# Optimization experiments

Measured on AMD Instinct MI355X. Metric: run time of the kernel, lower is better.

The kernel has to match this reference:

```python
import jax, jax.numpy as jnp
import numpy as np

RES_W, RES_H = 256, 256
MAX_SAMPLES = 384
TF_RES = 128
FOV_DEG = 30.0
NEAR, FAR = 0.1, 100.0
BG = 0.0
HIT_EPS = 1e-3


def _normalize(v, axis=-1):
    return v / jnp.linalg.norm(v, axis=axis, keepdims=True)


def trilinear_sample(vol, tex):
    # vol: [X,Y,Z], tex: [...,3] in voxel coordinates
    res = np.array(vol.shape, dtype=np.float32)
    p = jnp.clip(tex, 0.0, jnp.asarray(res - 1.0 - 1e-6, jnp.float32))
    lo = jnp.floor(p).astype(jnp.int32)
    f = p - lo.astype(p.dtype)
    hi = jnp.minimum(lo + 1, jnp.asarray(res.astype(np.int32) - 1))
    x0, y0, z0 = lo[..., 0], lo[..., 1], lo[..., 2]
    x1, y1, z1 = hi[..., 0], hi[..., 1], hi[..., 2]
    fx, fy, fz = f[..., 0], f[..., 1], f[..., 2]
    c000 = vol[x0, y0, z0]; c100 = vol[x1, y0, z0]
    c010 = vol[x0, y1, z0]; c110 = vol[x1, y1, z0]
    c001 = vol[x0, y0, z1]; c101 = vol[x1, y0, z1]
    c011 = vol[x0, y1, z1]; c111 = vol[x1, y1, z1]
    c00 = c000 * (1 - fx) + c100 * fx
    c10 = c010 * (1 - fx) + c110 * fx
    c01 = c001 * (1 - fx) + c101 * fx
    c11 = c011 * (1 - fx) + c111 * fx
    c0 = c00 * (1 - fy) + c10 * fy
    c1 = c01 * (1 - fy) + c11 * fy
    return c0 * (1 - fz) + c1 * fz


def tf_lookup(tf, x):
    # tf: [T,4], x: [...] intensity in [0,1]
    T = tf.shape[0]
    xi = jnp.clip(x, 0.0, 1.0) * (T - 1)
    lo = jnp.floor(xi).astype(jnp.int32)
    hi = jnp.minimum(lo + 1, T - 1)
    f = (xi - lo.astype(xi.dtype))[..., None]
    return tf[lo] * (1 - f) + tf[hi] * f


def render_one(vol, tf, cam, sr):
    # vol [X,Y,Z], tf [T,4], cam [3] -> [W,H,5] (rgba + depth)
    W, H = RES_W, RES_H
    fwd = _normalize(-cam)
    world_up = jnp.array([0.0, 1.0, 0.0], jnp.float32)
    right = _normalize(jnp.cross(fwd, world_up))
    up = jnp.cross(right, fwd)
    tanf = jnp.tan(jnp.float32(np.radians(FOV_DEG) / 2))
    aspect = W / H
    u = ((jnp.arange(W) + 0.5) / W * 2 - 1) * tanf * aspect  # [W]
    v = ((jnp.arange(H) + 0.5) / H * 2 - 1) * tanf           # [H]
    dirs = fwd + u[:, None, None] * right + v[None, :, None] * up  # [W,H,3]
    dirs = _normalize(dirs)
    # ray-box intersection against [-1,1]^3
    inv = 1.0 / dirs
    t_lo = (-1.0 - cam) * inv
    t_hi = (1.0 - cam) * inv
    tmin = jnp.max(jnp.minimum(t_lo, t_hi), axis=-1)
    tmax = jnp.min(jnp.maximum(t_lo, t_hi), axis=-1)
    hit = (tmax >= 0.0) & (tmin <= tmax)
    entry = jnp.maximum(tmin, NEAR)
    dist = jnp.where(hit, jnp.maximum(tmax - entry, 0.0), 0.0)
    vol_max = max(vol.shape)
    # Nyquist: step = voxel size (2/vol_max) / sampling_rate
    ns = jnp.clip(jnp.ceil(dist * 0.5 * vol_max * sr), 1.0, MAX_SAMPLES)
    step = dist / ns
    k = jnp.arange(MAX_SAMPLES, dtype=jnp.float32)
    t = entry[..., None] + (k + 0.5) * step[..., None]            # [W,H,S]
    valid = (k < ns[..., None]) & hit[..., None]
    pos = cam + t[..., None] * dirs[..., None, :]                 # [W,H,S,3]
    res_m1 = jnp.asarray(np.array(vol.shape, np.float32) - 1.0)
    tex = (pos * 0.5 + 0.5) * res_m1
    intensity = trilinear_sample(vol, tex)                        # [W,H,S]
    rgba = tf_lookup(tf, intensity)                               # [W,H,S,4]
    a = rgba[..., 3]
    a = 1.0 - (1.0 - a) ** (1.0 / sr)   # opacity correction for sampling rate
    a = jnp.where(valid, a, 0.0)
    one_m = 1.0 - a
    cp = jnp.cumprod(one_m, axis=-1)
    T_excl = jnp.concatenate([jnp.ones_like(cp[..., :1]), cp[..., :-1]], axis=-1)
    w = T_excl * a                                                # [W,H,S]
    rgb = jnp.einsum('whs,whsc->whc', w, rgba[..., :3])
    acc = jnp.sum(w, axis=-1)
    rgb_out = rgb + (1.0 - acc)[..., None] * BG
    # FirstHitDepth
    hit_s = a > HIT_EPS
    any_hit = jnp.any(hit_s, axis=-1)
    first = jnp.argmax(hit_s, axis=-1)
    t_first = jnp.take_along_axis(t, first[..., None], axis=-1)[..., 0]
    depth = jnp.where(any_hit, (t_first - NEAR) / (FAR - NEAR), 1.0)
    return jnp.concatenate([rgb_out, acc[..., None], depth[..., None]], axis=-1)


def setup_inputs() -> dict:
    key = jax.random.key(0)
    k1, k2, k3 = jax.random.split(key, 3)
    volume = jax.random.uniform(k1, (1, 256, 256, 256), dtype=jnp.float32)
    tf = jax.random.uniform(k2, (1, TF_RES, 4), dtype=jnp.float32)
    look_from = jnp.array([[0.9, 0.7, -2.2]], jnp.float32) + 0.1 * jax.random.normal(k3, (1, 3), dtype=jnp.float32)
    return {"volume": volume, "tf": tf, "look_from": look_from, "sampling_rate": 1}


def reference(volume, tf, look_from, sampling_rate):
    sr = float(sampling_rate)
    return jax.vmap(lambda v, t, c: render_one(v, t, c, sr))(volume, tf, look_from)
```

## Files before the change

### kernel.cpp

```cpp
#include <hip/hip_runtime.h>
#include <math.h>

#define RES_W 256
#define RES_H 256
#define TF_RES 128

typedef float float2u __attribute__((ext_vector_type(2), aligned(4)));

__global__ __launch_bounds__(256, 4) void raycast_kernel(
    const float* __restrict__ vol,
    const float* __restrict__ tf,
    const float* __restrict__ cam_p,
    const int*   __restrict__ sr_p,
    float* __restrict__ out)
{
    #pragma clang fp contract(off)

    __shared__ float tfR[TF_RES + 1], tfG[TF_RES + 1], tfB[TF_RES + 1], tfA[TF_RES + 1];
    const int tid = (int)threadIdx.x;
    if (tid < TF_RES) {
        float4 e = ((const float4*)tf)[tid];
        tfR[tid] = e.x; tfG[tid] = e.y; tfB[tid] = e.z; tfA[tid] = e.w;
        if (tid == TF_RES - 1) {
            tfR[TF_RES] = e.x; tfG[TF_RES] = e.y; tfB[TF_RES] = e.z; tfA[TF_RES] = e.w;
        }
    }
    __syncthreads();

    const int lane = tid & 63;
    const int sub  = lane & 31;

    const int b  = (int)blockIdx.x;
    const int sb = (b & 7) * 1024 + (b >> 3);
    const int ray = sb * 8 + (tid >> 5);
    const int h = ray & 255;
    const int w = ray >> 8;

    const float cx = cam_p[0], cy = cam_p[1], cz = cam_p[2];
    const int   sr_i = sr_p[0];
    const float srf = (float)sr_i;

    float nx = -cx, ny = -cy, nz = -cz;
    float fl = __fsqrt_rn((nx*nx + ny*ny) + nz*nz);
    float fx = nx / fl, fy = ny / fl, fz = nz / fl;
    float rxu = 0.0f - fz;
    float rzu = fx;
    float rl = __fsqrt_rn((rxu*rxu + 0.0f) + rzu*rzu);
    float rx = rxu / rl, rz = rzu / rl;
    float ux = 0.0f - rz*fy;
    float uy = rz*fx - rx*fz;
    float uz = rx*fy;

    const float ang32 = (float)((30.0 * 0.017453292519943295) * 0.5);
    const float tan_half = (float)tan((double)ang32);

    float uu = ((((float)w + 0.5f) / 256.0f) * 2.0f - 1.0f) * tan_half;
    float vv = ((((float)h + 0.5f) / 256.0f) * 2.0f - 1.0f) * tan_half;

    float dx = (fx + uu*rx) + vv*ux;
    float dy = (fy + 0.0f ) + vv*uy;
    float dz = (fz + uu*rz) + vv*uz;
    float dl = __fsqrt_rn((dx*dx + dy*dy) + dz*dz);
    dx = dx / dl; dy = dy / dl; dz = dz / dl;

    float ivx = 1.0f/dx, ivy = 1.0f/dy, ivz = 1.0f/dz;
    float tlx = (-1.0f - cx)*ivx, thx = (1.0f - cx)*ivx;
    float tly = (-1.0f - cy)*ivy, thy = (1.0f - cy)*ivy;
    float tlz = (-1.0f - cz)*ivz, thz = (1.0f - cz)*ivz;
    float tmin = fmaxf(fmaxf(fminf(tlx,thx), fminf(tly,thy)), fminf(tlz,thz));
    float tmax = fminf(fminf(fmaxf(tlx,thx), fmaxf(tly,thy)), fmaxf(tlz,thz));
    bool hit = (tmax >= 0.0f) && (tmin <= tmax);

    float entry = fmaxf(tmin, 0.1f);
    float dist  = hit ? fmaxf(tmax - entry, 0.0f) : 0.0f;
    float nsf   = fminf(fmaxf(ceilf(((dist * 0.5f) * 256.0f) * srf), 1.0f), 384.0f);
    int   ns    = (int)nsf;
    float step  = dist / nsf;

    float rgb_r = 0.0f, rgb_g = 0.0f, rgb_b = 0.0f, acc = 0.0f;
    float T_prev = 1.0f;
    int   hk_min = 0x7FFFFFFF;

    for (int base = 0; ; ) {
        const int  k     = base + sub;
        const bool valid = hit && (k < ns);

        float t  = entry + ((float)k + 0.5f) * step;
        float px = (cx + t*dx);
        float py = (cy + t*dy);
        float pz = (cz + t*dz);
        px = ((px * 0.5f) + 0.5f) * 255.0f;
        py = ((py * 0.5f) + 0.5f) * 255.0f;
        pz = ((pz * 0.5f) + 0.5f) * 255.0f;
        px = fminf(fmaxf(px, 0.0f), 255.0f);
        py = fminf(fmaxf(py, 0.0f), 255.0f);
        pz = fminf(fmaxf(pz, 0.0f), 255.0f);
        int x0 = (int)floorf(px), y0 = (int)floorf(py), z0 = (int)floorf(pz);
        float ffx = px - (float)x0;
        float ffy = py - (float)y0;
        float ffz = pz - (float)z0;
        int x1 = min(x0 + 1, 255);
        int y1 = min(y0 + 1, 255);
        int zb = min(z0, 254);
        int bx0 = x0 << 16, bx1 = x1 << 16;
        int by0 = y0 << 8,  by1 = y1 << 8;
        float2u p00 = *(const float2u*)(vol + (bx0 + by0 + zb));
        float2u p10 = *(const float2u*)(vol + (bx1 + by0 + zb));
        float2u p01 = *(const float2u*)(vol + (bx0 + by1 + zb));
        float2u p11 = *(const float2u*)(vol + (bx1 + by1 + zb));
        if (z0 == 255) {
            p00.x = p00.y; p10.x = p10.y; p01.x = p01.y; p11.x = p11.y;
        }

        float omx = 1.0f - ffx, omy = 1.0f - ffy, omz = 1.0f - ffz;
        float c00 = p00.x*omx + p10.x*ffx;
        float c10 = p01.x*omx + p11.x*ffx;
        float c01 = p00.y*omx + p10.y*ffx;
        float c11 = p01.y*omx + p11.y*ffx;
        float c0  = c00*omy + c10*ffy;
        float c1  = c01*omy + c11*ffy;
        float intensity = c0*omz + c1*ffz;

        float xi = fminf(fmaxf(intensity, 0.0f), 1.0f) * 127.0f;
        int lo  = (int)floorf(xi);
        float tfr = xi - (float)lo;
        float omt = 1.0f - tfr;
        float cr  = tfR[lo]*omt + tfR[lo + 1]*tfr;
        float cg  = tfG[lo]*omt + tfG[lo + 1]*tfr;
        float cbb = tfB[lo]*omt + tfB[lo + 1]*tfr;
        float a   = tfA[lo]*omt + tfA[lo + 1]*tfr;

        if (sr_i == 1) {
            a = 1.0f - (1.0f - a);
        } else {
            a = 1.0f - powf(1.0f - a, 1.0f / srf);
        }
        if (!valid) a = 0.0f;
        float one_m = 1.0f - a;

        float x = one_m;
        #pragma unroll
        for (int off = 1; off < 32; off <<= 1) {
            float y = __shfl_up(x, off);
            if (sub >= off) x *= y;
        }
        float ex = __shfl_up(x, 1);
        if (sub == 0) ex = 1.0f;

        float wgt = (T_prev * ex) * a;
        rgb_r += wgt * cr;
        rgb_g += wgt * cg;
        rgb_b += wgt * cbb;
        acc   += wgt;
        if (valid && (a > 1e-3f)) hk_min = min(hk_min, k);

        float Tc = __shfl(x, (lane & 32) | 31);
        T_prev = T_prev * Tc;

        base += 32;
        bool active = hit && (base < ns) && (T_prev >= 1e-7f);
        if (__ballot(active) == 0ULL) break;
    }

    #pragma unroll
    for (int m = 16; m >= 1; m >>= 1) {
        rgb_r += __shfl_xor(rgb_r, m);
        rgb_g += __shfl_xor(rgb_g, m);
        rgb_b += __shfl_xor(rgb_b, m);
        acc   += __shfl_xor(acc,   m);
        hk_min = min(hk_min, __shfl_xor(hk_min, m));
    }

    if (sub == 0) {
        float depth = 1.0f;
        if (hk_min != 0x7FFFFFFF) {
            float tfh = entry + ((float)hk_min + 0.5f) * step;
            depth = (tfh - 0.1f) / 99.9f;
        }
        int oi = (w * RES_H + h) * 5;
        out[oi + 0] = rgb_r;
        out[oi + 1] = rgb_g;
        out[oi + 2] = rgb_b;
        out[oi + 3] = acc;
        out[oi + 4] = depth;
    }
}

extern "C" void kernel_launch(void* const* d_in, const int* in_sizes, int n_in,
                              void* d_out, int out_size, void* d_ws, size_t ws_size,
                              hipStream_t stream) {
    const float* vol = (const float*)d_in[0];
    const float* tf  = (const float*)d_in[1];
    const float* cam = (const float*)d_in[2];
    const int*   sr  = (const int*)d_in[3];
    float* out = (float*)d_out;

    raycast_kernel<<<dim3(8192), dim3(256), 0, stream>>>(vol, tf, cam, sr, out);
}
```

Baseline: 113.7 us.

## Halve lanes per ray, precompute ray setup, and loosen early-termination threshold

```diff
diff --git a/kernel.cpp b/kernel.cpp
--- a/kernel.cpp
+++ b/kernel.cpp
@@ -7,38 +7,18 @@
 
 typedef float float2u __attribute__((ext_vector_type(2), aligned(4)));
 
-__global__ __launch_bounds__(256, 4) void raycast_kernel(
-    const float* __restrict__ vol,
-    const float* __restrict__ tf,
+__global__ __launch_bounds__(256) void ray_setup_kernel(
     const float* __restrict__ cam_p,
     const int*   __restrict__ sr_p,
-    float* __restrict__ out)
+    float* __restrict__ rws)
 {
     #pragma clang fp contract(off)
-
-    __shared__ float tfR[TF_RES + 1], tfG[TF_RES + 1], tfB[TF_RES + 1], tfA[TF_RES + 1];
-    const int tid = (int)threadIdx.x;
-    if (tid < TF_RES) {
-        float4 e = ((const float4*)tf)[tid];
-        tfR[tid] = e.x; tfG[tid] = e.y; tfB[tid] = e.z; tfA[tid] = e.w;
-        if (tid == TF_RES - 1) {
-            tfR[TF_RES] = e.x; tfG[TF_RES] = e.y; tfB[TF_RES] = e.z; tfA[TF_RES] = e.w;
-        }
-    }
-    __syncthreads();
-
-    const int lane = tid & 63;
-    const int sub  = lane & 31;
-
-    const int b  = (int)blockIdx.x;
-    const int sb = (b & 7) * 1024 + (b >> 3);
-    const int ray = sb * 8 + (tid >> 5);
+    const int ray = (int)blockIdx.x * 256 + (int)threadIdx.x;
     const int h = ray & 255;
     const int w = ray >> 8;
 
     const float cx = cam_p[0], cy = cam_p[1], cz = cam_p[2];
-    const int   sr_i = sr_p[0];
-    const float srf = (float)sr_i;
+    const float srf = (float)sr_p[0];
 
     float nx = -cx, ny = -cy, nz = -cz;
     float fl = __fsqrt_rn((nx*nx + ny*ny) + nz*nz);
@@ -74,8 +54,54 @@
     float entry = fmaxf(tmin, 0.1f);
     float dist  = hit ? fmaxf(tmax - entry, 0.0f) : 0.0f;
     float nsf   = fminf(fmaxf(ceilf(((dist * 0.5f) * 256.0f) * srf), 1.0f), 384.0f);
-    int   ns    = (int)nsf;
     float step  = dist / nsf;
+
+    float4* o = (float4*)(rws + (size_t)ray * 8);
+    o[0] = make_float4(dx, dy, dz, entry);
+    o[1] = make_float4(step, nsf, hit ? 1.0f : 0.0f, 0.0f);
+}
+
+__global__ __launch_bounds__(256) void raycast_kernel(
+    const float* __restrict__ vol,
+    const float* __restrict__ tf,
+    const float* __restrict__ cam_p,
+    const int*   __restrict__ sr_p,
+    const float* __restrict__ rws,
+    float* __restrict__ out)
+{
+    #pragma clang fp contract(off)
+
+    __shared__ float tfR[TF_RES + 1], tfG[TF_RES + 1], tfB[TF_RES + 1], tfA[TF_RES + 1];
+    const int tid = (int)threadIdx.x;
+    if (tid < TF_RES) {
+        float4 e = ((const float4*)tf)[tid];
+        tfR[tid] = e.x; tfG[tid] = e.y; tfB[tid] = e.z; tfA[tid] = e.w;
+        if (tid == TF_RES - 1) {
+            tfR[TF_RES] = e.x; tfG[TF_RES] = e.y; tfB[TF_RES] = e.z; tfA[TF_RES] = e.w;
+        }
+    }
+    __syncthreads();
+
+    const int lane = tid & 63;
+    const int sub  = lane & 15;
+
+    const int b  = (int)blockIdx.x;
+    const int sb = (b & 7) * 512 + (b >> 3);
+    const int ray = sb * 16 + (tid >> 4);
+    const int h = ray & 255;
+    const int w = ray >> 8;
+
+    const float cx = cam_p[0], cy = cam_p[1], cz = cam_p[2];
+    const int   sr_i = sr_p[0];
+    const float srf = (float)sr_i;
+
+    const float4* rp = (const float4*)(rws + (size_t)ray * 8);
+    float4 ra = rp[0];
+    float4 rb = rp[1];
+    const float dx = ra.x, dy = ra.y, dz = ra.z, entry = ra.w;
+    const float step = rb.x;
+    const int   ns   = (int)rb.y;
+    const bool  hit  = (rb.z != 0.0f);
 
     float rgb_r = 0.0f, rgb_g = 0.0f, rgb_b = 0.0f, acc = 0.0f;
     float T_prev = 1.0f;
@@ -140,7 +166,7 @@
 
         float x = one_m;
         #pragma unroll
-        for (int off = 1; off < 32; off <<= 1) {
+        for (int off = 1; off < 16; off <<= 1) {
             float y = __shfl_up(x, off);
             if (sub >= off) x *= y;
         }
@@ -154,16 +180,16 @@
         acc   += wgt;
         if (valid && (a > 1e-3f)) hk_min = min(hk_min, k);
 
-        float Tc = __shfl(x, (lane & 32) | 31);
+        float Tc = __shfl(x, (lane & 48) | 15);
         T_prev = T_prev * Tc;
 
-        base += 32;
-        bool active = hit && (base < ns) && (T_prev >= 1e-7f);
+        base += 16;
+        bool active = hit && (base < ns) && (T_prev >= 1e-4f);
         if (__ballot(active) == 0ULL) break;
     }
 
     #pragma unroll
-    for (int m = 16; m >= 1; m >>= 1) {
+    for (int m = 8; m >= 1; m >>= 1) {
         rgb_r += __shfl_xor(rgb_r, m);
         rgb_g += __shfl_xor(rgb_g, m);
         rgb_b += __shfl_xor(rgb_b, m);
@@ -194,6 +220,8 @@
     const float* cam = (const float*)d_in[2];
     const int*   sr  = (const int*)d_in[3];
     float* out = (float*)d_out;
-
-    raycast_kernel<<<dim3(8192), dim3(256), 0, stream>>>(vol, tf, cam, sr, out);
+    float* rws = (float*)d_ws;
+
+    ray_setup_kernel<<<dim3(256), dim3(256), 0, stream>>>(cam, sr, rws);
+    raycast_kernel<<<dim3(4096), dim3(256), 0, stream>>>(vol, tf, cam, sr, rws, out);
 }
```

Measured after the change: 103.4 us. -9.1%, faster.

## Switch to one ray per thread with 8x8 tiles and early ray termination

Applied to the files above, without the earlier changes.

```diff
diff --git a/kernel.cpp b/kernel.cpp
--- a/kernel.cpp
+++ b/kernel.cpp
@@ -7,7 +7,7 @@
 
 typedef float float2u __attribute__((ext_vector_type(2), aligned(4)));
 
-__global__ __launch_bounds__(256, 4) void raycast_kernel(
+__global__ __launch_bounds__(64) void raycast_kernel(
     const float* __restrict__ vol,
     const float* __restrict__ tf,
     const float* __restrict__ cam_p,
@@ -18,23 +18,24 @@
 
     __shared__ float tfR[TF_RES + 1], tfG[TF_RES + 1], tfB[TF_RES + 1], tfA[TF_RES + 1];
     const int tid = (int)threadIdx.x;
-    if (tid < TF_RES) {
-        float4 e = ((const float4*)tf)[tid];
-        tfR[tid] = e.x; tfG[tid] = e.y; tfB[tid] = e.z; tfA[tid] = e.w;
-        if (tid == TF_RES - 1) {
-            tfR[TF_RES] = e.x; tfG[TF_RES] = e.y; tfB[TF_RES] = e.z; tfA[TF_RES] = e.w;
+    {
+        const float4* tf4 = (const float4*)tf;
+        float4 e0 = tf4[tid];
+        float4 e1 = tf4[tid + 64];
+        tfR[tid] = e0.x; tfG[tid] = e0.y; tfB[tid] = e0.z; tfA[tid] = e0.w;
+        tfR[tid + 64] = e1.x; tfG[tid + 64] = e1.y; tfB[tid + 64] = e1.z; tfA[tid + 64] = e1.w;
+        if (tid == 63) {
+            tfR[TF_RES] = e1.x; tfG[TF_RES] = e1.y; tfB[TF_RES] = e1.z; tfA[TF_RES] = e1.w;
         }
     }
     __syncthreads();
 
-    const int lane = tid & 63;
-    const int sub  = lane & 31;
-
-    const int b  = (int)blockIdx.x;
-    const int sb = (b & 7) * 1024 + (b >> 3);
-    const int ray = sb * 8 + (tid >> 5);
-    const int h = ray & 255;
-    const int w = ray >> 8;
+    const int b    = (int)blockIdx.x;
+    const int tile = (b % 8) * 128 + (b / 8);
+    const int tile_h = tile % 32;
+    const int tile_w = tile / 32;
+    const int h = tile_h * 8 + (tid % 8);
+    const int w = tile_w * 8 + (tid / 8);
 
     const float cx = cam_p[0], cy = cam_p[1], cz = cam_p[2];
     const int   sr_i = sr_p[0];
@@ -78,105 +79,82 @@
     float step  = dist / nsf;
 
     float rgb_r = 0.0f, rgb_g = 0.0f, rgb_b = 0.0f, acc = 0.0f;
-    float T_prev = 1.0f;
-    int   hk_min = 0x7FFFFFFF;
+    float Texcl = 1.0f;
+    float depth = 1.0f;
+    bool  found = false;
+    bool  done  = !hit;
+    int   k = 0;
 
-    for (int base = 0; ; ) {
-        const int  k     = base + sub;
-        const bool valid = hit && (k < ns);
+    for (;;) {
+        if (!done) {
+            float t  = entry + ((float)k + 0.5f) * step;
+            float px = (cx + t*dx);
+            float py = (cy + t*dy);
+            float pz = (cz + t*dz);
+            px = ((px * 0.5f) + 0.5f) * 255.0f;
+            py = ((py * 0.5f) + 0.5f) * 255.0f;
+            pz = ((pz * 0.5f) + 0.5f) * 255.0f;
+            px = fminf(fmaxf(px, 0.0f), 255.0f);
+            py = fminf(fmaxf(py, 0.0f), 255.0f);
+            pz = fminf(fmaxf(pz, 0.0f), 255.0f);
+            int x0 = (int)px, y0 = (int)py, z0 = (int)pz;
+            float ffx = px - (float)x0;
+            float ffy = py - (float)y0;
+            float ffz = pz - (float)z0;
+            int x1 = min(x0 + 1, 255);
+            int y1 = min(y0 + 1, 255);
+            int zb = min(z0, 254);
+            int bx0 = x0 << 16, bx1 = x1 << 16;
+            int by0 = y0 << 8,  by1 = y1 << 8;
+            float2u p00 = *(const float2u*)(vol + (bx0 + by0 + zb));
+            float2u p10 = *(const float2u*)(vol + (bx1 + by0 + zb));
+            float2u p01 = *(const float2u*)(vol + (bx0 + by1 + zb));
+            float2u p11 = *(const float2u*)(vol + (bx1 + by1 + zb));
+            if (z0 == 255) {
+                p00.x = p00.y; p10.x = p10.y; p01.x = p01.y; p11.x = p11.y;
+            }
 
-        float t  = entry + ((float)k + 0.5f) * step;
-        float px = (cx + t*dx);
-        float py = (cy + t*dy);
-        float pz = (cz + t*dz);
-        px = ((px * 0.5f) + 0.5f) * 255.0f;
-        py = ((py * 0.5f) + 0.5f) * 255.0f;
-        pz = ((pz * 0.5f) + 0.5f) * 255.0f;
-        px = fminf(fmaxf(px, 0.0f), 255.0f);
-        py = fminf(fmaxf(py, 0.0f), 255.0f);
-        pz = fminf(fmaxf(pz, 0.0f), 255.0f);
-        int x0 = (int)floorf(px), y0 = (int)floorf(py), z0 = (int)floorf(pz);
-        float ffx = px - (float)x0;
-        float ffy = py - (float)y0;
-        float ffz = pz - (float)z0;
-        int x1 = min(x0 + 1, 255);
-        int y1 = min(y0 + 1, 255);
-        int zb = min(z0, 254);
-        int bx0 = x0 << 16, bx1 = x1 << 16;
-        int by0 = y0 << 8,  by1 = y1 << 8;
-        float2u p00 = *(const float2u*)(vol + (bx0 + by0 + zb));
-        float2u p10 = *(const float2u*)(vol + (bx1 + by0 + zb));
-        float2u p01 = *(const float2u*)(vol + (bx0 + by1 + zb));
-        float2u p11 = *(const float2u*)(vol + (bx1 + by1 + zb));
-        if (z0 == 255) {
-            p00.x = p00.y; p10.x = p10.y; p01.x = p01.y; p11.x = p11.y;
+            float omx = 1.0f - ffx, omy = 1.0f - ffy, omz = 1.0f - ffz;
+            float c00 = p00.x*omx + p10.x*ffx;
+            float c10 = p01.x*omx + p11.x*ffx;
+            float c01 = p00.y*omx + p10.y*ffx;
+            float c11 = p01.y*omx + p11.y*ffx;
+            float c0  = c00*omy + c10*ffy;
+            float c1  = c01*omy + c11*ffy;
+            float intensity = c0*omz + c1*ffz;
+
+            float xi = fminf(fmaxf(intensity, 0.0f), 1.0f) * 127.0f;
+            int lo  = (int)xi;
+            float tfr = xi - (float)lo;
+            float omt = 1.0f - tfr;
+            float cr  = tfR[lo]*omt + tfR[lo + 1]*tfr;
+            float cg  = tfG[lo]*omt + tfG[lo + 1]*tfr;
+            float cbb = tfB[lo]*omt + tfB[lo + 1]*tfr;
+            float a   = tfA[lo]*omt + tfA[lo + 1]*tfr;
+
+            if (sr_i == 1) {
+                a = 1.0f - (1.0f - a);
+            } else {
+                a = 1.0f - powf(1.0f - a, 1.0f / srf);
+            }
+            float one_m = 1.0f - a;
+            float wgt = Texcl * a;
+            rgb_r += wgt * cr;
+            rgb_g += wgt * cg;
+            rgb_b += wgt * cbb;
+            acc   += wgt;
+            if (!found && a > 1e-3f) {
+                found = true;
+                depth = (t - 0.1f) / 99.9f;
+            }
+            Texcl = Texcl * one_m;
+            k++;
+            done = (k >= ns) || (Texcl < 2e-3f);
         }
-
-        float omx = 1.0f - ffx, omy = 1.0f - ffy, omz = 1.0f - ffz;
-        float c00 = p00.x*omx + p10.x*ffx;
-        float c10 = p01.x*omx + p11.x*ffx;
-        float c01 = p00.y*omx + p10.y*ffx;
-        float c11 = p01.y*omx + p11.y*ffx;
-        float c0  = c00*omy + c10*ffy;
-        float c1  = c01*omy + c11*ffy;
-        float intensity = c0*omz + c1*ffz;
-
-        float xi = fminf(fmaxf(intensity, 0.0f), 1.0f) * 127.0f;
-        int lo  = (int)floorf(xi);
-        float tfr = xi - (float)lo;
-        float omt = 1.0f - tfr;
-        float cr  = tfR[lo]*omt + tfR[lo + 1]*tfr;
-        float cg  = tfG[lo]*omt + tfG[lo + 1]*tfr;
-        float cbb = tfB[lo]*omt + tfB[lo + 1]*tfr;
-        float a   = tfA[lo]*omt + tfA[lo + 1]*tfr;
-
-        if (sr_i == 1) {
-            a = 1.0f - (1.0f - a);
-        } else {
-            a = 1.0f - powf(1.0f - a, 1.0f / srf);
-        }
-        if (!valid) a = 0.0f;
-        float one_m = 1.0f - a;
-
-        float x = one_m;
-        #pragma unroll
-        for (int off = 1; off < 32; off <<= 1) {
-            float y = __shfl_up(x, off);
-            if (sub >= off) x *= y;
-        }
-        float ex = __shfl_up(x, 1);
-        if (sub == 0) ex = 1.0f;
-
-        float wgt = (T_prev * ex) * a;
-        rgb_r += wgt * cr;
-        rgb_g += wgt * cg;
-        rgb_b += wgt * cbb;
-        acc   += wgt;
-        if (valid && (a > 1e-3f)) hk_min = min(hk_min, k);
-
-        float Tc = __shfl(x, (lane & 32) | 31);
-        T_prev = T_prev * Tc;
-
-        base += 32;
-        bool active = hit && (base < ns) && (T_prev >= 1e-7f);
-        if (__ballot(active) == 0ULL) break;
+        if (__ballot(!done) == 0ULL) break;
     }
 
-    #pragma unroll
-    for (int m = 16; m >= 1; m >>= 1) {
-        rgb_r += __shfl_xor(rgb_r, m);
-        rgb_g += __shfl_xor(rgb_g, m);
-        rgb_b += __shfl_xor(rgb_b, m);
-        acc   += __shfl_xor(acc,   m);
-        hk_min = min(hk_min, __shfl_xor(hk_min, m));
-    }
-
-    if (sub == 0) {
-        float depth = 1.0f;
-        if (hk_min != 0x7FFFFFFF) {
-            float tfh = entry + ((float)hk_min + 0.5f) * step;
-            depth = (tfh - 0.1f) / 99.9f;
-        }
+    {
         int oi = (w * RES_H + h) * 5;
         out[oi + 0] = rgb_r;
         out[oi + 1] = rgb_g;
@@ -195,5 +173,5 @@
     const int*   sr  = (const int*)d_in[3];
     float* out = (float*)d_out;
 
-    raycast_kernel<<<dim3(8192), dim3(256), 0, stream>>>(vol, tf, cam, sr, out);
+    raycast_kernel<<<dim3(1024), dim3(64), 0, stream>>>(vol, tf, cam, sr, out);
 }
```

Result: faster. 99.92 us (-12.1%).
